# Kernel tuning notes

Hardware: AMD Instinct MI355X
Metric: run time of the kernel (lower is better)

The kernel has to match this reference:

```python
import jax, jax.numpy as jnp
import numpy as np

SEARCH_RANGE = 4  # max_displacement == pad in tfa CorrelationCost


def setup_inputs() -> dict:
    key = jax.random.key(0)
    k1, k2 = jax.random.split(key)
    B, C, H, W = 4, 128, 128, 256
    prv = jax.random.normal(k1, (B, C, H, W), dtype=jnp.float32)
    nxt = jax.random.normal(k2, (B, C, H, W), dtype=jnp.float32)
    return {"prv": prv, "nxt": nxt}


def reference(prv, nxt):
    """tfa CorrelationCost with kernel_size=1, stride_1=stride_2=1,
    max_displacement=pad=SEARCH_RANGE, channels_first.

    out[b, k, y, x] = (1/C) * sum_c prv[b,c,y,x] * nxt_pad[b,c,y+dy,x+dx]
    with k = (dy+d)*(2d+1) + (dx+d) (dy outer loop, dx inner, as in the
    tfa CUDA kernel), nxt zero-padded by d on each spatial side.
    """
    d = SEARCH_RANGE
    B, C, H, W = prv.shape
    nd = 2 * d + 1  # neighborhood width -> nd*nd output channels
    nxt_pad = jnp.pad(nxt, ((0, 0), (0, 0), (d, d), (d, d)))
    inv_c = jnp.float32(1.0 / C)
    outs = []
    # fixed small loop over (2d+1)^2 = 81 displacement offsets
    for dy in range(nd):
        for dx in range(nd):
            shifted = jax.lax.dynamic_slice(nxt_pad, (0, 0, dy, dx), (B, C, H, W))
            # reduce over channels: [B, H, W]
            outs.append(jnp.einsum('bchw,bchw->bhw', prv, shifted) * inv_c)
    return jnp.stack(outs, axis=1)  # [B, 81, H, W]
```

## Files before the change

### kernel.cpp

```cpp
#include <hip/hip_runtime.h>


#define SR 4
#define ND 9
#define BB 4
#define CC 128
#define HH 128
#define WW 256
#define HW (HH * WW)
#define PADW (WW + 8)

typedef __fp16 h2 __attribute__((ext_vector_type(2)));

static __device__ __forceinline__ h2 pk(float lo, float hi) {
    return __builtin_amdgcn_cvt_pkrtz(lo, hi);
}
static __device__ __forceinline__ h2 as_h2(unsigned int u) {
    union { unsigned int u; h2 h; } v; v.u = u; return v.h;
}
static __device__ __forceinline__ unsigned int as_u32(h2 h) {
    union { unsigned int u; h2 h; } v; v.h = h; return v.u;
}

#define CFENCE asm volatile("" ::: "memory")

__global__ __launch_bounds__(256) void costvol_kernel(
    const float* __restrict__ prv,
    const float* __restrict__ nxt,
    float* __restrict__ out)
{
    __shared__ unsigned int lds[4][2][PADW];

    const int nwg  = gridDim.x;
    const int cpx  = nwg >> 3;
    const int orig = blockIdx.x;
    const int wid  = (orig & 7) * cpx + (orig >> 3);

    const int dy = wid % ND;
    const int r  = wid / ND;
    const int y4 = r & 31;
    const int b  = r >> 5;

    const int tid  = threadIdx.x;
    const int ry   = tid >> 6;
    const int lane = tid & 63;
    const int x0   = lane << 2;
    const int y    = (y4 << 2) + ry;
    const int yp   = y + dy - SR;

    float* outp = out + (((size_t)b * (ND * ND) + (size_t)dy * ND) * HH + y) * WW + x0;

    if (yp < 0 || yp >= HH) {
        const float4 z = make_float4(0.f, 0.f, 0.f, 0.f);
        #pragma unroll
        for (int dx = 0; dx < ND; ++dx)
            *reinterpret_cast<float4*>(outp + (size_t)dx * HW) = z;
        return;
    }

    const float* pg = prv + ((size_t)b * CC * HH + y)  * WW + x0;
    const float* ng = nxt + ((size_t)b * CC * HH + yp) * WW + x0;

    if (lane < 2) {
        const uint4 z = make_uint4(0u, 0u, 0u, 0u);
        *reinterpret_cast<uint4*>(&lds[ry][lane][0])      = z;
        *reinterpret_cast<uint4*>(&lds[ry][lane][WW + 4]) = z;
    }

    float acc[ND][4];
    #pragma unroll
    for (int dx = 0; dx < ND; ++dx)
        #pragma unroll
        for (int j = 0; j < 4; ++j)
            acc[dx][j] = 0.f;

    uint4* st0 = reinterpret_cast<uint4*>(&lds[ry][0][4 + x0]);
    uint4* st1 = reinterpret_cast<uint4*>(&lds[ry][1][4 + x0]);
    const uint4* rl0 = reinterpret_cast<const uint4*>(&lds[ry][0][x0]);
    const uint4* rr0 = reinterpret_cast<const uint4*>(&lds[ry][0][x0 + 8]);
    const uint4* rl1 = reinterpret_cast<const uint4*>(&lds[ry][1][x0]);
    const uint4* rr1 = reinterpret_cast<const uint4*>(&lds[ry][1][x0 + 8]);

    auto dotp = [&](const h2* ph, const uint4 wlu, const h2* own, const uint4 wru) {
        h2 n12[12];
        n12[0]  = as_h2(wlu.x); n12[1]  = as_h2(wlu.y);
        n12[2]  = as_h2(wlu.z); n12[3]  = as_h2(wlu.w);
        n12[4]  = own[0]; n12[5] = own[1]; n12[6] = own[2]; n12[7] = own[3];
        n12[8]  = as_h2(wru.x); n12[9]  = as_h2(wru.y);
        n12[10] = as_h2(wru.z); n12[11] = as_h2(wru.w);
        #pragma unroll
        for (int dx = 0; dx < ND; ++dx)
            #pragma unroll
            for (int j = 0; j < 4; ++j)
                acc[dx][j] = __builtin_amdgcn_fdot2(ph[j], n12[dx + j], acc[dx][j], false);
    };

    #define GLD(P0, P1, N0, N1) do { \
        P0 = *reinterpret_cast<const float4*>(pg); \
        P1 = *reinterpret_cast<const float4*>(pg + HW); pg += 2 * HW; \
        N0 = *reinterpret_cast<const float4*>(ng); \
        N1 = *reinterpret_cast<const float4*>(ng + HW); ng += 2 * HW; } while (0)

    #define CVTN(NH, N0, N1) do { \
        NH[0] = pk(N0.x, N1.x); NH[1] = pk(N0.y, N1.y); \
        NH[2] = pk(N0.z, N1.z); NH[3] = pk(N0.w, N1.w); } while (0)

    #define STORE4(ST, NH) do { uint4 t_; \
        t_.x = as_u32(NH[0]); t_.y = as_u32(NH[1]); \
        t_.z = as_u32(NH[2]); t_.w = as_u32(NH[3]); *(ST) = t_; } while (0)

    #define DOT(PP0, PP1, WLC, NH_OWN, WRC) do { \
        h2 ph_[4]; \
        ph_[0] = pk(PP0.x, PP1.x); ph_[1] = pk(PP0.y, PP1.y); \
        ph_[2] = pk(PP0.z, PP1.z); ph_[3] = pk(PP0.w, PP1.w); \
        dotp(ph_, WLC, NH_OWN, WRC); } while (0)

    #define PHASE(ST, NS0, NS1, NH_ST, GP0, GP1, GN0, GN1, \
                  RL, RR, WLN, WRN, PP0, PP1, NH_OWN, WLC, WRC) do { \
        CVTN(NH_ST, NS0, NS1); STORE4(ST, NH_ST); \
        GLD(GP0, GP1, GN0, GN1); \
        CFENCE; \
        WLN = *(RL); WRN = *(RR); \
        CFENCE; \
        DOT(PP0, PP1, WLC, NH_OWN, WRC); } while (0)

    float4 pA0, pA1, nA0, nA1, pB0, pB1, nB0, nB1;
    float4 pC0, pC1, nC0, nC1, pD0, pD1, nD0, nD1;
    h2 nhA[4], nhB[4], nhC[4], nhD[4];
    uint4 wlX, wrX, wlY, wrY;

    GLD(pA0, pA1, nA0, nA1);
    GLD(pB0, pB1, nB0, nB1);
    GLD(pC0, pC1, nC0, nC1);
    CVTN(nhA, nA0, nA1); STORE4(st0, nhA);
    CFENCE;
    wlX = *rl0; wrX = *rr0;
    CFENCE;

    for (int k = 0; k < 60; k += 4) {
        PHASE(st1, nB0, nB1, nhB, pD0, pD1, nD0, nD1,
              rl1, rr1, wlY, wrY, pA0, pA1, nhA, wlX, wrX);
        PHASE(st0, nC0, nC1, nhC, pA0, pA1, nA0, nA1,
              rl0, rr0, wlX, wrX, pB0, pB1, nhB, wlY, wrY);
        PHASE(st1, nD0, nD1, nhD, pB0, pB1, nB0, nB1,
              rl1, rr1, wlY, wrY, pC0, pC1, nhC, wlX, wrX);
        PHASE(st0, nA0, nA1, nhA, pC0, pC1, nC0, nC1,
              rl0, rr0, wlX, wrX, pD0, pD1, nhD, wlY, wrY);
    }
    {
        CVTN(nhB, nB0, nB1); STORE4(st1, nhB);
        GLD(pD0, pD1, nD0, nD1);
        CFENCE;
        wlY = *rl1; wrY = *rr1;
        CFENCE;
        DOT(pA0, pA1, wlX, nhA, wrX);
        CVTN(nhC, nC0, nC1); STORE4(st0, nhC);
        CFENCE;
        wlX = *rl0; wrX = *rr0;
        CFENCE;
        DOT(pB0, pB1, wlY, nhB, wrY);
        CVTN(nhD, nD0, nD1); STORE4(st1, nhD);
        CFENCE;
        wlY = *rl1; wrY = *rr1;
        CFENCE;
        DOT(pC0, pC1, wlX, nhC, wrX);
        DOT(pD0, pD1, wlY, nhD, wrY);
    }
    #undef PHASE
    #undef DOT
    #undef STORE4
    #undef CVTN
    #undef GLD

    const float invc = 1.0f / (float)CC;
    #pragma unroll
    for (int dx = 0; dx < ND; ++dx) {
        const float4 o = make_float4(acc[dx][0] * invc, acc[dx][1] * invc,
                                     acc[dx][2] * invc, acc[dx][3] * invc);
        *reinterpret_cast<float4*>(outp + (size_t)dx * HW) = o;
    }
}

extern "C" void kernel_launch(void* const* d_in, const int* in_sizes, int n_in,
                              void* d_out, int out_size, void* d_ws, size_t ws_size,
                              hipStream_t stream) {
    const float* prv = (const float*)d_in[0];
    const float* nxt = (const float*)d_in[1];
    float* out = (float*)d_out;

    const int nblocks = BB * (HH / 4) * ND;
    costvol_kernel<<<nblocks, 256, 0, stream>>>(prv, nxt, out);
}
```

Before: 57.50 us.

## Split channel reduction across wave pairs with LDS cross-wave reduction

Each block now covers 2 output rows instead of 4. The four waves are split as 2 rows × 2 channel halves, so each wave reduces over 64 channels rather than 128, and the two partial sums are combined through shared memory before the store. This doubles the block count and halves the serial per-wave channel loop, which should improve latency hiding and load balance. The cost is two __syncthreads, an LDS round-trip for the partials, and keeping waves whose rows fall outside the image alive until the barrier.

```diff
diff --git a/kernel.cpp b/kernel.cpp
--- a/kernel.cpp
+++ b/kernel.cpp
@@ -29,43 +29,29 @@
     const float* __restrict__ nxt,
     float* __restrict__ out)
 {
-    __shared__ unsigned int lds[4][2][PADW];
+    __shared__ __align__(16) unsigned int shraw[2 * 64 * 36];
 
     const int nwg  = gridDim.x;
     const int cpx  = nwg >> 3;
     const int orig = blockIdx.x;
     const int wid  = (orig & 7) * cpx + (orig >> 3);
 
-    const int dy = wid % ND;
-    const int r  = wid / ND;
-    const int y4 = r & 31;
-    const int b  = r >> 5;
+    const int dy  = wid % ND;
+    const int r   = wid / ND;
+    const int yp2 = r & 63;
+    const int b   = r >> 6;
 
     const int tid  = threadIdx.x;
-    const int ry   = tid >> 6;
+    const int w    = tid >> 6;
     const int lane = tid & 63;
+    const int ry   = w & 1;
+    const int ch   = w >> 1;
     const int x0   = lane << 2;
-    const int y    = (y4 << 2) + ry;
-    const int yp   = y + dy - SR;
-
-    float* outp = out + (((size_t)b * (ND * ND) + (size_t)dy * ND) * HH + y) * WW + x0;
-
-    if (yp < 0 || yp >= HH) {
-        const float4 z = make_float4(0.f, 0.f, 0.f, 0.f);
-        #pragma unroll
-        for (int dx = 0; dx < ND; ++dx)
-            *reinterpret_cast<float4*>(outp + (size_t)dx * HW) = z;
-        return;
-    }
-
-    const float* pg = prv + ((size_t)b * CC * HH + y)  * WW + x0;
-    const float* ng = nxt + ((size_t)b * CC * HH + yp) * WW + x0;
-
-    if (lane < 2) {
-        const uint4 z = make_uint4(0u, 0u, 0u, 0u);
-        *reinterpret_cast<uint4*>(&lds[ry][lane][0])      = z;
-        *reinterpret_cast<uint4*>(&lds[ry][lane][WW + 4]) = z;
-    }
+    const int y    = (yp2 << 1) + ry;
+    const int yq   = y + dy - SR;
+    const int c0   = ch << 6;
+
+    const bool valid = (yq >= 0) && (yq < HH);
 
     float acc[ND][4];
     #pragma unroll
@@ -74,110 +60,145 @@
         for (int j = 0; j < 4; ++j)
             acc[dx][j] = 0.f;
 
-    uint4* st0 = reinterpret_cast<uint4*>(&lds[ry][0][4 + x0]);
-    uint4* st1 = reinterpret_cast<uint4*>(&lds[ry][1][4 + x0]);
-    const uint4* rl0 = reinterpret_cast<const uint4*>(&lds[ry][0][x0]);
-    const uint4* rr0 = reinterpret_cast<const uint4*>(&lds[ry][0][x0 + 8]);
-    const uint4* rl1 = reinterpret_cast<const uint4*>(&lds[ry][1][x0]);
-    const uint4* rr1 = reinterpret_cast<const uint4*>(&lds[ry][1][x0 + 8]);
-
-    auto dotp = [&](const h2* ph, const uint4 wlu, const h2* own, const uint4 wru) {
-        h2 n12[12];
-        n12[0]  = as_h2(wlu.x); n12[1]  = as_h2(wlu.y);
-        n12[2]  = as_h2(wlu.z); n12[3]  = as_h2(wlu.w);
-        n12[4]  = own[0]; n12[5] = own[1]; n12[6] = own[2]; n12[7] = own[3];
-        n12[8]  = as_h2(wru.x); n12[9]  = as_h2(wru.y);
-        n12[10] = as_h2(wru.z); n12[11] = as_h2(wru.w);
-        #pragma unroll
-        for (int dx = 0; dx < ND; ++dx)
+    if (valid) {
+        const float* pg = prv + ((size_t)(b * CC + c0)) * HW + y  * WW + x0;
+        const float* ng = nxt + ((size_t)(b * CC + c0)) * HW + yq * WW + x0;
+
+        unsigned int* stage = shraw + w * (2 * PADW);
+
+        if (lane < 2) {
+            const uint4 z = make_uint4(0u, 0u, 0u, 0u);
+            *reinterpret_cast<uint4*>(stage + lane * PADW)          = z;
+            *reinterpret_cast<uint4*>(stage + lane * PADW + WW + 4) = z;
+        }
+
+        unsigned int* st0 = stage + 0 * PADW + 4 + x0;
+        unsigned int* st1 = stage + 1 * PADW + 4 + x0;
+        const uint4* rl0 = reinterpret_cast<const uint4*>(stage + 0 * PADW + x0);
+        const uint4* rr0 = reinterpret_cast<const uint4*>(stage + 0 * PADW + x0 + 8);
+        const uint4* rl1 = reinterpret_cast<const uint4*>(stage + 1 * PADW + x0);
+        const uint4* rr1 = reinterpret_cast<const uint4*>(stage + 1 * PADW + x0 + 8);
+
+        auto dotp = [&](const h2* ph, const uint4 wlu, const h2* own, const uint4 wru) {
+            h2 n12[12];
+            n12[0]  = as_h2(wlu.x); n12[1]  = as_h2(wlu.y);
+            n12[2]  = as_h2(wlu.z); n12[3]  = as_h2(wlu.w);
+            n12[4]  = own[0]; n12[5] = own[1]; n12[6] = own[2]; n12[7] = own[3];
+            n12[8]  = as_h2(wru.x); n12[9]  = as_h2(wru.y);
+            n12[10] = as_h2(wru.z); n12[11] = as_h2(wru.w);
             #pragma unroll
-            for (int j = 0; j < 4; ++j)
-                acc[dx][j] = __builtin_amdgcn_fdot2(ph[j], n12[dx + j], acc[dx][j], false);
-    };
-
-    #define GLD(P0, P1, N0, N1) do { \
-        P0 = *reinterpret_cast<const float4*>(pg); \
-        P1 = *reinterpret_cast<const float4*>(pg + HW); pg += 2 * HW; \
-        N0 = *reinterpret_cast<const float4*>(ng); \
-        N1 = *reinterpret_cast<const float4*>(ng + HW); ng += 2 * HW; } while (0)
-
-    #define CVTN(NH, N0, N1) do { \
-        NH[0] = pk(N0.x, N1.x); NH[1] = pk(N0.y, N1.y); \
-        NH[2] = pk(N0.z, N1.z); NH[3] = pk(N0.w, N1.w); } while (0)
-
-    #define STORE4(ST, NH) do { uint4 t_; \
-        t_.x = as_u32(NH[0]); t_.y = as_u32(NH[1]); \
-        t_.z = as_u32(NH[2]); t_.w = as_u32(NH[3]); *(ST) = t_; } while (0)
-
-    #define DOT(PP0, PP1, WLC, NH_OWN, WRC) do { \
-        h2 ph_[4]; \
-        ph_[0] = pk(PP0.x, PP1.x); ph_[1] = pk(PP0.y, PP1.y); \
-        ph_[2] = pk(PP0.z, PP1.z); ph_[3] = pk(PP0.w, PP1.w); \
-        dotp(ph_, WLC, NH_OWN, WRC); } while (0)
-
-    #define PHASE(ST, NS0, NS1, NH_ST, GP0, GP1, GN0, GN1, \
-                  RL, RR, WLN, WRN, PP0, PP1, NH_OWN, WLC, WRC) do { \
-        CVTN(NH_ST, NS0, NS1); STORE4(ST, NH_ST); \
-        GLD(GP0, GP1, GN0, GN1); \
-        CFENCE; \
-        WLN = *(RL); WRN = *(RR); \
-        CFENCE; \
-        DOT(PP0, PP1, WLC, NH_OWN, WRC); } while (0)
-
-    float4 pA0, pA1, nA0, nA1, pB0, pB1, nB0, nB1;
-    float4 pC0, pC1, nC0, nC1, pD0, pD1, nD0, nD1;
-    h2 nhA[4], nhB[4], nhC[4], nhD[4];
-    uint4 wlX, wrX, wlY, wrY;
-
-    GLD(pA0, pA1, nA0, nA1);
-    GLD(pB0, pB1, nB0, nB1);
-    GLD(pC0, pC1, nC0, nC1);
-    CVTN(nhA, nA0, nA1); STORE4(st0, nhA);
-    CFENCE;
-    wlX = *rl0; wrX = *rr0;
-    CFENCE;
-
-    for (int k = 0; k < 60; k += 4) {
-        PHASE(st1, nB0, nB1, nhB, pD0, pD1, nD0, nD1,
-              rl1, rr1, wlY, wrY, pA0, pA1, nhA, wlX, wrX);
-        PHASE(st0, nC0, nC1, nhC, pA0, pA1, nA0, nA1,
-              rl0, rr0, wlX, wrX, pB0, pB1, nhB, wlY, wrY);
-        PHASE(st1, nD0, nD1, nhD, pB0, pB1, nB0, nB1,
-              rl1, rr1, wlY, wrY, pC0, pC1, nhC, wlX, wrX);
-        PHASE(st0, nA0, nA1, nhA, pC0, pC1, nC0, nC1,
-              rl0, rr0, wlX, wrX, pD0, pD1, nhD, wlY, wrY);
-    }
-    {
-        CVTN(nhB, nB0, nB1); STORE4(st1, nhB);
-        GLD(pD0, pD1, nD0, nD1);
-        CFENCE;
-        wlY = *rl1; wrY = *rr1;
-        CFENCE;
-        DOT(pA0, pA1, wlX, nhA, wrX);
-        CVTN(nhC, nC0, nC1); STORE4(st0, nhC);
+            for (int dx = 0; dx < ND; ++dx)
+                #pragma unroll
+                for (int j = 0; j < 4; ++j)
+                    acc[dx][j] = __builtin_amdgcn_fdot2(ph[j], n12[dx + j], acc[dx][j], false);
+        };
+
+        #define GLD(P0, P1, N0, N1) do { \
+            P0 = *reinterpret_cast<const float4*>(pg); \
+            P1 = *reinterpret_cast<const float4*>(pg + HW); pg += 2 * HW; \
+            N0 = *reinterpret_cast<const float4*>(ng); \
+            N1 = *reinterpret_cast<const float4*>(ng + HW); ng += 2 * HW; } while (0)
+
+        #define CVTN(NH, N0, N1) do { \
+            NH[0] = pk(N0.x, N1.x); NH[1] = pk(N0.y, N1.y); \
+            NH[2] = pk(N0.z, N1.z); NH[3] = pk(N0.w, N1.w); } while (0)
+
+        #define STORE4(ST, NH) do { uint4 t_; \
+            t_.x = as_u32(NH[0]); t_.y = as_u32(NH[1]); \
+            t_.z = as_u32(NH[2]); t_.w = as_u32(NH[3]); \
+            *reinterpret_cast<uint4*>(ST) = t_; } while (0)
+
+        #define DOT(PP0, PP1, WLC, NH_OWN, WRC) do { \
+            h2 ph_[4]; \
+            ph_[0] = pk(PP0.x, PP1.x); ph_[1] = pk(PP0.y, PP1.y); \
+            ph_[2] = pk(PP0.z, PP1.z); ph_[3] = pk(PP0.w, PP1.w); \
+            dotp(ph_, WLC, NH_OWN, WRC); } while (0)
+
+        #define PHASE(ST, NS0, NS1, NH_ST, GP0, GP1, GN0, GN1, \
+                      RL, RR, WLN, WRN, PP0, PP1, NH_OWN, WLC, WRC) do { \
+            CVTN(NH_ST, NS0, NS1); STORE4(ST, NH_ST); \
+            GLD(GP0, GP1, GN0, GN1); \
+            CFENCE; \
+            WLN = *(RL); WRN = *(RR); \
+            CFENCE; \
+            DOT(PP0, PP1, WLC, NH_OWN, WRC); } while (0)
+
+        float4 pA0, pA1, nA0, nA1, pB0, pB1, nB0, nB1;
+        float4 pC0, pC1, nC0, nC1, pD0, pD1, nD0, nD1;
+        h2 nhA[4], nhB[4], nhC[4], nhD[4];
+        uint4 wlX, wrX, wlY, wrY;
+
+        GLD(pA0, pA1, nA0, nA1);
+        GLD(pB0, pB1, nB0, nB1);
+        GLD(pC0, pC1, nC0, nC1);
+        CVTN(nhA, nA0, nA1); STORE4(st0, nhA);
         CFENCE;
         wlX = *rl0; wrX = *rr0;
         CFENCE;
-        DOT(pB0, pB1, wlY, nhB, wrY);
-        CVTN(nhD, nD0, nD1); STORE4(st1, nhD);
-        CFENCE;
-        wlY = *rl1; wrY = *rr1;
-        CFENCE;
-        DOT(pC0, pC1, wlX, nhC, wrX);
-        DOT(pD0, pD1, wlY, nhD, wrY);
+
+        for (int k = 0; k < 28; k += 4) {
+            PHASE(st1, nB0, nB1, nhB, pD0, pD1, nD0, nD1,
+                  rl1, rr1, wlY, wrY, pA0, pA1, nhA, wlX, wrX);
+            PHASE(st0, nC0, nC1, nhC, pA0, pA1, nA0, nA1,
+                  rl0, rr0, wlX, wrX, pB0, pB1, nhB, wlY, wrY);
+            PHASE(st1, nD0, nD1, nhD, pB0, pB1, nB0, nB1,
+                  rl1, rr1, wlY, wrY, pC0, pC1, nhC, wlX, wrX);
+            PHASE(st0, nA0, nA1, nhA, pC0, pC1, nC0, nC1,
+                  rl0, rr0, wlX, wrX, pD0, pD1, nhD, wlY, wrY);
+        }
+        {
+            CVTN(nhB, nB0, nB1); STORE4(st1, nhB);
+            GLD(pD0, pD1, nD0, nD1);
+            CFENCE;
+            wlY = *rl1; wrY = *rr1;
+            CFENCE;
+            DOT(pA0, pA1, wlX, nhA, wrX);
+
+            CVTN(nhC, nC0, nC1); STORE4(st0, nhC);
+            CFENCE;
+            wlX = *rl0; wrX = *rr0;
+            CFENCE;
+            DOT(pB0, pB1, wlY, nhB, wrY);
+
+            CVTN(nhD, nD0, nD1); STORE4(st1, nhD);
+            CFENCE;
+            wlY = *rl1; wrY = *rr1;
+            CFENCE;
+            DOT(pC0, pC1, wlX, nhC, wrX);
+
+            DOT(pD0, pD1, wlY, nhD, wrY);
+        }
+        #undef PHASE
+        #undef DOT
+        #undef STORE4
+        #undef CVTN
+        #undef GLD
     }
-    #undef PHASE
-    #undef DOT
-    #undef STORE4
-    #undef CVTN
-    #undef GLD
-
-    const float invc = 1.0f / (float)CC;
-    #pragma unroll
-    for (int dx = 0; dx < ND; ++dx) {
-        const float4 o = make_float4(acc[dx][0] * invc, acc[dx][1] * invc,
-                                     acc[dx][2] * invc, acc[dx][3] * invc);
-        *reinterpret_cast<float4*>(outp + (size_t)dx * HW) = o;
+
+    __syncthreads();
+    if (ch == 1) {
+        float* red = reinterpret_cast<float*>(shraw) + ry * (64 * 36) + lane * 36;
+        #pragma unroll
+        for (int dx = 0; dx < ND; ++dx) {
+            float4 t = make_float4(acc[dx][0], acc[dx][1], acc[dx][2], acc[dx][3]);
+            *reinterpret_cast<float4*>(red + dx * 4) = t;
+        }
+    }
+    __syncthreads();
+    if (ch == 0) {
+        const float* red = reinterpret_cast<const float*>(shraw) + ry * (64 * 36) + lane * 36;
+        float* outp = out + (((size_t)b * (ND * ND) + (size_t)dy * ND) * HH + y) * WW + x0;
+        const float invc = 1.0f / (float)CC;
+        #pragma unroll
+        for (int dx = 0; dx < ND; ++dx) {
+            const float4 t = *reinterpret_cast<const float4*>(red + dx * 4);
+            float4 o;
+            o.x = (acc[dx][0] + t.x) * invc;
+            o.y = (acc[dx][1] + t.y) * invc;
+            o.z = (acc[dx][2] + t.z) * invc;
+            o.w = (acc[dx][3] + t.w) * invc;
+            *reinterpret_cast<float4*>(outp + (size_t)dx * HW) = o;
+        }
     }
 }
 
@@ -188,6 +209,6 @@
     const float* nxt = (const float*)d_in[1];
     float* out = (float*)d_out;
 
-    const int nblocks = BB * (HH / 4) * ND;
+    const int nblocks = BB * (HH / 2) * ND;
     costvol_kernel<<<nblocks, 256, 0, stream>>>(prv, nxt, out);
 }
```

Result: no change. 56.55 us (-1.7%).
